# Performance work log

Measured on AMD Instinct MI355X. Metric: run time of the kernel, lower is better.

## Reference

```python
import jax, jax.numpy as jnp
import numpy as np

EPS = 1e-5

def _cfn(x, g, b):
    # ChanFreqNorm: normalize over (channel, freq) dims of [B, C, T, F]
    mu = x.mean(axis=(1, 3), keepdims=True)
    std = jnp.sqrt(((x - mu) ** 2).mean(axis=(1, 3), keepdims=True))  # unbiased=False
    return (x - mu) / (std + EPS) * g[None, :, None, :] + b[None, :, None, :]

def _branch(x, w, bi, a, g, be):
    # 1x1 conv (C_in -> C_out) + PReLU(scalar) + ChanFreqNorm
    y = jnp.einsum('bctf,oc->botf', x, w) + bi[None, :, None, None]
    y = jnp.where(y > 0, y, a * y)
    return _cfn(y, g, be)


def setup_inputs() -> dict:
    key = jax.random.key(0)
    ks = jax.random.split(key, 8)
    B, C, T, F = 8, 64, 1000, 64
    H, HS, CV = 4, 4, 16  # num_heads, hidden_size, C // num_heads
    s = 0.05
    inp = {
        'x': jax.random.normal(ks[0], (B, C, T, F), jnp.float32),
        'q_w': jax.random.normal(ks[1], (H, HS, C), jnp.float32) * s,
        'q_b': jnp.zeros((H, HS), jnp.float32),
        'q_a': jnp.full((H,), 0.25, jnp.float32),
        'q_g': jnp.ones((H, HS, F), jnp.float32),
        'q_be': jnp.zeros((H, HS, F), jnp.float32),
        'k_w': jax.random.normal(ks[2], (H, HS, C), jnp.float32) * s,
        'k_b': jnp.zeros((H, HS), jnp.float32),
        'k_a': jnp.full((H,), 0.25, jnp.float32),
        'k_g': jnp.ones((H, HS, F), jnp.float32),
        'k_be': jnp.zeros((H, HS, F), jnp.float32),
        'v_w': jax.random.normal(ks[3], (H, CV, C), jnp.float32) * s,
        'v_b': jnp.zeros((H, CV), jnp.float32),
        'v_a': jnp.full((H,), 0.25, jnp.float32),
        'v_g': jnp.ones((H, CV, F), jnp.float32),
        'v_be': jnp.zeros((H, CV, F), jnp.float32),
        'l_w': jax.random.normal(ks[4], (C, C), jnp.float32) * s,
        'l_b': jnp.zeros((C,), jnp.float32),
        'l_a': jnp.full((1,), 0.25, jnp.float32),
        'l_g': jnp.ones((C, F), jnp.float32),
        'l_be': jnp.zeros((C, F), jnp.float32),
    }
    return inp


def reference(x, q_w, q_b, q_a, q_g, q_be, k_w, k_b, k_a, k_g, k_be,
              v_w, v_b, v_a, v_g, v_be, l_w, l_b, l_a, l_g, l_be):
    B, C, T, F = x.shape
    H = q_w.shape[0]
    branch = jax.vmap(_branch, in_axes=(None, 0, 0, 0, 0, 0))
    Q = branch(x, q_w, q_b, q_a, q_g, q_be)   # [H, B, HS, T, F]
    K = branch(x, k_w, k_b, k_a, k_g, k_be)   # [H, B, HS, T, F]
    V = branch(x, v_w, v_b, v_a, v_g, v_be)   # [H, B, CV, T, F]
    HS = Q.shape[2]
    CV = V.shape[2]
    HB = H * B
    # torch.cat(dim=0) over heads == head-major reshape
    Ql = Q.reshape(HB, HS, T, F).transpose(0, 2, 1, 3).reshape(HB, T, HS * F)
    Kl = K.reshape(HB, HS, T, F).transpose(0, 2, 1, 3).reshape(HB, T, HS * F)
    Vl = V.reshape(HB, CV, T, F).transpose(0, 2, 1, 3).reshape(HB, T, CV * F)
    embed_size = H * F  # num_heads * num_freqs
    scores = jnp.einsum('ntd,nsd->nts', Ql, Kl) / jnp.sqrt(jnp.float32(embed_size))
    attn = jax.nn.softmax(scores, axis=-1)               # [HB, T, T]
    A = jnp.einsum('nts,nsd->ntd', attn, Vl)             # [HB, T, CV*F]
    A = A.reshape(HB, T, CV, F).transpose(0, 2, 1, 3)    # [HB, CV, T, F]
    xo = A.reshape(H, B, CV, T, F).transpose(1, 0, 2, 3, 4).reshape(B, C, T, F)
    y = jnp.einsum('bctf,oc->botf', xo, l_w) + l_b[None, :, None, None]
    y = jnp.where(y > 0, y, l_a[0] * y)
    y = _cfn(y, l_g, l_be)
    return y + x
```

## Files before the change

### kernel.cpp

```cpp
#include <hip/hip_runtime.h>
#include <hip/hip_bf16.h>

typedef __hip_bfloat16 bf16;
typedef __attribute__((ext_vector_type(8))) short bf16x8;
typedef __attribute__((ext_vector_type(4))) float f32x4;

#define TT 1000
#define SCALE 0.0625f
#define M0 20.0f
#define KSR 264
#define PSR 72
#define XSC 68

__device__ __forceinline__ float b2f(const bf16 v) { return __bfloat162float(v); }
__device__ __forceinline__ bf16 f2b(const float v) { return __float2bfloat16(v); }
__device__ __forceinline__ unsigned short f2bu(float v) { bf16 h = __float2bfloat16(v); return *(unsigned short*)&h; }
__device__ __forceinline__ float u2f(unsigned short u) { return __bfloat162float(*(const bf16*)&u); }

__global__ __launch_bounds__(256, 2) void k_qkv(
    const float* __restrict__ x,
    const float* __restrict__ qw, const float* __restrict__ qb, const float* __restrict__ qa,
    const float* __restrict__ qg, const float* __restrict__ qbe,
    const float* __restrict__ kw, const float* __restrict__ kb, const float* __restrict__ ka,
    const float* __restrict__ kg, const float* __restrict__ kbe,
    const float* __restrict__ vw, const float* __restrict__ vb, const float* __restrict__ va,
    const float* __restrict__ vg, const float* __restrict__ vbe,
    bf16* __restrict__ Ql, bf16* __restrict__ Kl, bf16* __restrict__ Vl)
{
    __shared__ float Xs[2][64][XSC];
    __shared__ uint4 Whs[12 * 64];
    __shared__ uint4 Wls[12 * 64];
    __shared__ float gs_s[2][12][4];
    __shared__ float gq_s[2][12][4];
    __shared__ float bias_s[96];
    __shared__ float alpha_s[24];

    const int tid  = threadIdx.x;
    const int b    = blockIdx.x / 125;
    const int ch   = blockIdx.x % 125;
    const int tb   = ch * 8;

    const int w    = tid >> 6;
    const int lane = tid & 63;
    const int cl   = lane & 15;
    const int oct  = lane >> 4;
    const int f    = w * 16 + cl;

    #pragma unroll
    for (int i = 0; i < 3; ++i) {
        const int s  = w * 3 + i;
        const int mt = s >> 1, kk = s & 1;
        const int row = mt * 16 + cl;
        const float* wp = (row < 16) ? (qw + row * 64)
                        : (row < 32) ? (kw + (row - 16) * 64)
                                     : (vw + (row - 32) * 64);
        const int c0 = kk * 32 + oct * 8;
        const float4 a0 = *(const float4*)(wp + c0);
        const float4 a1 = *(const float4*)(wp + c0 + 4);
        const float vvv[8] = {a0.x, a0.y, a0.z, a0.w, a1.x, a1.y, a1.z, a1.w};
        union { unsigned short u[8]; uint4 q; } hi, lo;
        #pragma unroll
        for (int j = 0; j < 8; ++j) {
            const unsigned short h = f2bu(vvv[j]);
            hi.u[j] = h;
            lo.u[j] = f2bu(vvv[j] - u2f(h));
        }
        Whs[s * 64 + lane] = hi.q;
        Wls[s * 64 + lane] = lo.q;
    }
    if (tid < 96) {
        const int r = tid;
        bias_s[r] = (r < 16) ? qb[r] : (r < 32) ? kb[r - 16] : vb[r - 32];
    }
    if (tid < 24) {
        const int mt = tid >> 2, oc = tid & 3;
        alpha_s[tid] = (mt == 0) ? qa[oc] : (mt == 1) ? ka[oc] : va[mt - 2];
    }

    float g_r[24], be_r[24];
    #pragma unroll
    for (int mt = 0; mt < 6; ++mt)
        #pragma unroll
        for (int r = 0; r < 4; ++r) {
            const int row = mt * 16 + oct * 4 + r;
            const float* gp; const float* bp; int rr;
            if (row < 16)      { rr = row;      gp = qg; bp = qbe; }
            else if (row < 32) { rr = row - 16; gp = kg; bp = kbe; }
            else               { rr = row - 32; gp = vg; bp = vbe; }
            g_r[mt * 4 + r]  = gp[rr * 64 + f];
            be_r[mt * 4 + r] = bp[rr * 64 + f];
        }

    auto stageX = [&](int t0) {
        const int c = lane;
        #pragma unroll
        for (int tt = 0; tt < 2; ++tt) {
            const float* xp = x + ((size_t)(b * 64 + c) * TT + (t0 + tt)) * 64 + w * 16;
            const float4 v0 = *(const float4*)(xp);
            const float4 v1 = *(const float4*)(xp + 4);
            const float4 v2 = *(const float4*)(xp + 8);
            const float4 v3 = *(const float4*)(xp + 12);
            const float vv[16] = {v0.x, v0.y, v0.z, v0.w, v1.x, v1.y, v1.z, v1.w,
                                  v2.x, v2.y, v2.z, v2.w, v3.x, v3.y, v3.z, v3.w};
            #pragma unroll
            for (int j = 0; j < 16; ++j) Xs[tt][w * 16 + j][c] = vv[j];
        }
    };

    stageX(tb);
    __syncthreads();

    for (int it = 0; it < 4; ++it) {
        const int t0 = tb + it * 2;

        f32x4 acc[2][6];
        #pragma unroll
        for (int tt = 0; tt < 2; ++tt)
            #pragma unroll
            for (int mt = 0; mt < 6; ++mt) acc[tt][mt] = (f32x4)0.f;

        #pragma unroll
        for (int tt = 0; tt < 2; ++tt) {
            #pragma unroll
            for (int kk = 0; kk < 2; ++kk) {
                const float* xr = &Xs[tt][w * 16 + cl][kk * 32 + oct * 8];
                const float4 x0 = *(const float4*)(xr);
                const float4 x1 = *(const float4*)(xr + 4);
                const float xvv[8] = {x0.x, x0.y, x0.z, x0.w, x1.x, x1.y, x1.z, x1.w};
                union { unsigned short u[8]; bf16x8 v; } xh, xl;
                #pragma unroll
                for (int j = 0; j < 8; ++j) {
                    const unsigned short h = f2bu(xvv[j]);
                    xh.u[j] = h;
                    xl.u[j] = f2bu(xvv[j] - u2f(h));
                }
                #pragma unroll
                for (int mt = 0; mt < 6; ++mt) {
                    const bf16x8 wh = *(const bf16x8*)&Whs[(mt * 2 + kk) * 64 + lane];
                    const bf16x8 wl = *(const bf16x8*)&Wls[(mt * 2 + kk) * 64 + lane];
                    acc[tt][mt] = __builtin_amdgcn_mfma_f32_16x16x32_bf16(wh, xh.v, acc[tt][mt], 0, 0, 0);
                    acc[tt][mt] = __builtin_amdgcn_mfma_f32_16x16x32_bf16(wh, xl.v, acc[tt][mt], 0, 0, 0);
                    acc[tt][mt] = __builtin_amdgcn_mfma_f32_16x16x32_bf16(wl, xh.v, acc[tt][mt], 0, 0, 0);
                }
            }
        }

        #pragma unroll
        for (int tt = 0; tt < 2; ++tt)
            #pragma unroll
            for (int mt = 0; mt < 6; ++mt) {
                float s = 0.f, q = 0.f;
                #pragma unroll
                for (int r = 0; r < 4; ++r) {
                    float v = acc[tt][mt][r] + bias_s[mt * 16 + oct * 4 + r];
                    const float a = alpha_s[mt * 4 + oct];
                    v = v > 0.f ? v : a * v;
                    acc[tt][mt][r] = v;
                    s += v; q += v * v;
                }
                s += __shfl_xor(s, 1); q += __shfl_xor(q, 1);
                s += __shfl_xor(s, 2); q += __shfl_xor(q, 2);
                s += __shfl_xor(s, 4); q += __shfl_xor(q, 4);
                s += __shfl_xor(s, 8); q += __shfl_xor(q, 8);
                if (mt < 2) {
                    if (cl == 0) { gs_s[tt][mt * 4 + oct][w] = s; gq_s[tt][mt * 4 + oct][w] = q; }
                } else {
                    s += __shfl_xor(s, 16); q += __shfl_xor(q, 16);
                    s += __shfl_xor(s, 32); q += __shfl_xor(q, 32);
                    if (lane == 0) { gs_s[tt][8 + mt - 2][w] = s; gq_s[tt][8 + mt - 2][w] = q; }
                }
            }
        __syncthreads();

        #pragma unroll
        for (int tt = 0; tt < 2; ++tt) {
            const int t = t0 + tt;
            #pragma unroll
            for (int mt = 0; mt < 6; ++mt) {
                const int g = (mt < 2) ? (mt * 4 + oct) : (8 + mt - 2);
                const float s = gs_s[tt][g][0] + gs_s[tt][g][1] + gs_s[tt][g][2] + gs_s[tt][g][3];
                const float q = gq_s[tt][g][0] + gq_s[tt][g][1] + gq_s[tt][g][2] + gq_s[tt][g][3];
                const float cnt = (mt < 2) ? 256.f : 1024.f;
                const float mu = s / cnt;
                const float var = fmaxf(q / cnt - mu * mu, 0.f);
                const float sc = 1.f / (sqrtf(var) + 1e-5f);
                #pragma unroll
                for (int r = 0; r < 4; ++r) {
                    const float out = (acc[tt][mt][r] - mu) * sc * g_r[mt * 4 + r] + be_r[mt * 4 + r];
                    if (mt == 0) {
                        Ql[((size_t)(oct * 8 + b) * TT + t) * 256 + r * 64 + f] = f2b(out);
                    } else if (mt == 1) {
                        Kl[((size_t)(oct * 8 + b) * TT + t) * 256 + r * 64 + f] = f2b(out);
                    } else {
                        Vl[((size_t)((mt - 2) * 8 + b) * TT + t) * 1024 + (oct * 4 + r) * 64 + f] = f2b(out);
                    }
                }
            }
        }

        if (it < 3) stageX(tb + (it + 1) * 2);
        __syncthreads();
    }
}

__global__ __launch_bounds__(256, 2) void k_vt(
    const unsigned short* __restrict__ Vl, unsigned short* __restrict__ Vt)
{
    __shared__ unsigned short Ts[64 * 80];
    const int tid = threadIdx.x;
    const int n  = blockIdx.x >> 8;
    const int tt = (blockIdx.x >> 4) & 15;
    const int dt = blockIdx.x & 15;
    const int t0 = tt * 64, d0 = dt * 64;

    #pragma unroll
    for (int i = 0; i < 2; ++i) {
        const int chunk = tid + i * 256;
        const int trow = chunk >> 3, tc8 = (chunk & 7) * 8;
        uint4 v = make_uint4(0u, 0u, 0u, 0u);
        const int t = t0 + trow;
        if (t < TT) v = *(const uint4*)&Vl[((size_t)n * TT + t) * 1024 + d0 + tc8];
        *(uint4*)&Ts[trow * 80 + tc8] = v;
    }
    __syncthreads();
    #pragma unroll
    for (int i = 0; i < 2; ++i) {
        const int chunk = tid + i * 256;
        const int drow = chunk >> 3, sc8 = (chunk & 7) * 8;
        union { unsigned short u[8]; uint4 v; } pk;
        #pragma unroll
        for (int j = 0; j < 8; ++j) pk.u[j] = Ts[(sc8 + j) * 80 + drow];
        *(uint4*)&Vt[((size_t)n * 1024 + d0 + drow) * 1024 + t0 + sc8] = pk.v;
    }
}

__global__ __launch_bounds__(512, 2) void k_attn(
    const unsigned short* __restrict__ Ql, const unsigned short* __restrict__ Kl,
    const unsigned short* __restrict__ Vt, bf16* __restrict__ Aout)
{
    __shared__ unsigned short Qs[64 * KSR];
    __shared__ unsigned short Ks[64 * KSR];
    __shared__ unsigned short Ps[64 * PSR];
    __shared__ float lred[8][32];
    __shared__ float invl[64];

    const int tid  = threadIdx.x;
    const int bid  = blockIdx.x;
    const int xcd  = bid & 7;
    const int r0   = bid >> 3;
    const int n    = xcd * 4 + (r0 >> 4);
    const int t0   = (r0 & 15) * 64;
    const int valid_r = TT - t0;

    const int w    = tid >> 6;
    const int lane = tid & 63;
    const int cl   = lane & 15;
    const int oct  = lane >> 4;

    const int qh   = w & 1;
    const int sw   = w >> 1;

    #pragma unroll
    for (int i = 0; i < 4; ++i) {
        const int chunk = tid + i * 512;
        const int row = chunk >> 5, c8 = (chunk & 31) * 8;
        uint4 v = make_uint4(0u, 0u, 0u, 0u);
        if (row < valid_r)
            v = *(const uint4*)&Ql[((size_t)n * TT + t0 + row) * 256 + c8];
        *(uint4*)&Qs[row * KSR + c8] = v;
    }
    #pragma unroll
    for (int i = 0; i < 4; ++i) {
        const int chunk = tid + i * 512;
        const int row = chunk >> 5, c8 = (chunk & 31) * 8;
        uint4 v = make_uint4(0u, 0u, 0u, 0u);
        if (row < TT)
            v = *(const uint4*)&Kl[((size_t)n * TT + row) * 256 + c8];
        *(uint4*)&Ks[row * KSR + c8] = v;
    }
    __syncthreads();

    f32x4 acc[4][8];
    #pragma unroll
    for (int qt = 0; qt < 4; ++qt)
        #pragma unroll
        for (int dt = 0; dt < 8; ++dt) acc[qt][dt] = (f32x4)0.f;
    float l_acc[2][4] = {{0.f,0.f,0.f,0.f},{0.f,0.f,0.f,0.f}};

    for (int ts = 0; ts < 16; ++ts) {
        const int s0 = ts * 64;

        f32x4 sacc0 = (f32x4)0.f, sacc1 = (f32x4)0.f;
        #pragma unroll
        for (int k = 0; k < 8; ++k) {
            const bf16x8 bk  = *(const bf16x8*)&Ks[(sw * 16 + cl) * KSR + k * 32 + oct * 8];
            const bf16x8 aq0 = *(const bf16x8*)&Qs[(qh * 32 + cl) * KSR + k * 32 + oct * 8];
            const bf16x8 aq1 = *(const bf16x8*)&Qs[(qh * 32 + 16 + cl) * KSR + k * 32 + oct * 8];
            sacc0 = __builtin_amdgcn_mfma_f32_16x16x32_bf16(aq0, bk, sacc0, 0, 0, 0);
            sacc1 = __builtin_amdgcn_mfma_f32_16x16x32_bf16(aq1, bk, sacc1, 0, 0, 0);
        }
        const float msk = (s0 + sw * 16 + cl < TT) ? 1.f : 0.f;
        #pragma unroll
        for (int r = 0; r < 4; ++r) {
            const float p0 = msk * __expf(sacc0[r] * SCALE - M0);
            const float p1 = msk * __expf(sacc1[r] * SCALE - M0);
            l_acc[0][r] += p0;
            l_acc[1][r] += p1;
            Ps[(qh * 32 + oct * 4 + r) * PSR + sw * 16 + cl] = f2bu(p0);
            Ps[(qh * 32 + 16 + oct * 4 + r) * PSR + sw * 16 + cl] = f2bu(p1);
        }
        __syncthreads();

        const int s0n = s0 + 64;
        uint4 kv[2];
        if (ts < 15) {
            #pragma unroll
            for (int i = 0; i < 2; ++i) {
                const int chunk = tid + i * 512;
                const int row = chunk >> 5, c8 = (chunk & 31) * 8;
                kv[i] = make_uint4(0u, 0u, 0u, 0u);
                if (s0n + row < TT)
                    kv[i] = *(const uint4*)&Kl[((size_t)n * TT + s0n + row) * 256 + c8];
            }
        }

        bf16x8 pa[4][2];
        #pragma unroll
        for (int qt = 0; qt < 4; ++qt)
            #pragma unroll
            for (int kc = 0; kc < 2; ++kc)
                pa[qt][kc] = *(const bf16x8*)&Ps[(qt * 16 + cl) * PSR + kc * 32 + oct * 8];

        const unsigned short* vbase =
            Vt + ((size_t)n * 1024 + w * 128 + cl) * 1024 + s0 + oct * 8;

        {
            bf16x8 vb[4][2];
            #pragma unroll
            for (int dt = 0; dt < 4; ++dt) {
                const unsigned short* vp = vbase + (size_t)(dt * 16) * 1024;
                vb[dt][0] = *(const bf16x8*)(vp);
                vb[dt][1] = *(const bf16x8*)(vp + 32);
            }
            #pragma unroll
            for (int dt = 0; dt < 4; ++dt)
                #pragma unroll
                for (int qt = 0; qt < 4; ++qt) {
                    acc[qt][dt] = __builtin_amdgcn_mfma_f32_16x16x32_bf16(pa[qt][0], vb[dt][0], acc[qt][dt], 0, 0, 0);
                    acc[qt][dt] = __builtin_amdgcn_mfma_f32_16x16x32_bf16(pa[qt][1], vb[dt][1], acc[qt][dt], 0, 0, 0);
                }
        }

        if (ts < 15) {
            #pragma unroll
            for (int i = 0; i < 2; ++i) {
                const int chunk = tid + i * 512;
                const int row = chunk >> 5, c8 = (chunk & 31) * 8;
                *(uint4*)&Ks[row * KSR + c8] = kv[i];
            }
            #pragma unroll
            for (int i = 2; i < 4; ++i) {
                const int chunk = tid + i * 512;
                const int row = chunk >> 5, c8 = (chunk & 31) * 8;
                kv[i - 2] = make_uint4(0u, 0u, 0u, 0u);
                if (s0n + row < TT)
                    kv[i - 2] = *(const uint4*)&Kl[((size_t)n * TT + s0n + row) * 256 + c8];
            }
        }

        {
            bf16x8 vb[4][2];
            #pragma unroll
            for (int dt = 0; dt < 4; ++dt) {
                const unsigned short* vp = vbase + (size_t)((dt + 4) * 16) * 1024;
                vb[dt][0] = *(const bf16x8*)(vp);
                vb[dt][1] = *(const bf16x8*)(vp + 32);
            }
            #pragma unroll
            for (int dt = 0; dt < 4; ++dt)
                #pragma unroll
                for (int qt = 0; qt < 4; ++qt) {
                    acc[qt][dt + 4] = __builtin_amdgcn_mfma_f32_16x16x32_bf16(pa[qt][0], vb[dt][0], acc[qt][dt + 4], 0, 0, 0);
                    acc[qt][dt + 4] = __builtin_amdgcn_mfma_f32_16x16x32_bf16(pa[qt][1], vb[dt][1], acc[qt][dt + 4], 0, 0, 0);
                }
        }

        if (ts < 15) {
            #pragma unroll
            for (int i = 2; i < 4; ++i) {
                const int chunk = tid + i * 512;
                const int row = chunk >> 5, c8 = (chunk & 31) * 8;
                *(uint4*)&Ks[row * KSR + c8] = kv[i - 2];
            }
        }
        __syncthreads();
    }

    #pragma unroll
    for (int u = 0; u < 2; ++u)
        #pragma unroll
        for (int r = 0; r < 4; ++r) {
            float l = l_acc[u][r];
            l += __shfl_xor(l, 1); l += __shfl_xor(l, 2);
            l += __shfl_xor(l, 4); l += __shfl_xor(l, 8);
            l_acc[u][r] = l;
        }
    if (cl == 0) {
        #pragma unroll
        for (int u = 0; u < 2; ++u)
            #pragma unroll
            for (int r = 0; r < 4; ++r)
                lred[w][u * 16 + oct * 4 + r] = l_acc[u][r];
    }
    __syncthreads();
    if (tid < 64) {
        const int qhh = tid >> 5, rh = tid & 31;
        invl[tid] = 1.f / (lred[qhh][rh] + lred[qhh + 2][rh] +
                           lred[qhh + 4][rh] + lred[qhh + 6][rh]);
    }
    __syncthreads();

    #pragma unroll
    for (int qt = 0; qt < 4; ++qt)
        #pragma unroll
        for (int r = 0; r < 4; ++r) {
            const int row = qt * 16 + oct * 4 + r;
            if (row < valid_r) {
                bf16* op = Aout + ((size_t)n * TT + t0 + row) * 1024 + w * 128 + cl;
                const float iv = invl[row];
                #pragma unroll
                for (int dt = 0; dt < 8; ++dt)
                    op[dt * 16] = f2b(acc[qt][dt][r] * iv);
            }
        }
}

__global__ __launch_bounds__(256, 2) void k_final(
    const bf16* __restrict__ Ain, const float* __restrict__ x,
    const float* __restrict__ lw, const float* __restrict__ lb, const float* __restrict__ la,
    const float* __restrict__ lg, const float* __restrict__ lbe,
    float* __restrict__ out)
{
    __shared__ float Xs[2][64][XSC];
    __shared__ uint4 Whs[8 * 64];
    __shared__ uint4 Wls[8 * 64];
    __shared__ float red_s[2][2][4];
    __shared__ float bias_s[64];

    const int tid  = threadIdx.x;
    const int b    = blockIdx.x / 125;
    const int ch   = blockIdx.x % 125;
    const int tb   = ch * 8;

    const int w    = tid >> 6;
    const int lane = tid & 63;
    const int cl   = lane & 15;
    const int oct  = lane >> 4;
    const int f    = w * 16 + cl;

    #pragma unroll
    for (int i = 0; i < 2; ++i) {
        const int s  = w * 2 + i;
        const int mt = s >> 1, kk = s & 1;
        const float* wp = lw + (mt * 16 + cl) * 64 + kk * 32 + oct * 8;
        const float4 a0 = *(const float4*)(wp);
        const float4 a1 = *(const float4*)(wp + 4);
        const float vvv[8] = {a0.x, a0.y, a0.z, a0.w, a1.x, a1.y, a1.z, a1.w};
        union { unsigned short u[8]; uint4 q; } hi, lo;
        #pragma unroll
        for (int j = 0; j < 8; ++j) {
            const unsigned short h = f2bu(vvv[j]);
            hi.u[j] = h;
            lo.u[j] = f2bu(vvv[j] - u2f(h));
        }
        Whs[s * 64 + lane] = hi.q;
        Wls[s * 64 + lane] = lo.q;
    }
    if (tid < 64) bias_s[tid] = lb[tid];
    const float alpha = la[0];

    float g_r[16], be_r[16];
    #pragma unroll
    for (int mt = 0; mt < 4; ++mt)
        #pragma unroll
        for (int r = 0; r < 4; ++r) {
            const int rr = mt * 16 + oct * 4 + r;
            g_r[mt * 4 + r]  = lg[rr * 64 + f];
            be_r[mt * 4 + r] = lbe[rr * 64 + f];
        }

    auto stageA = [&](int t0) {
        #pragma unroll
        for (int tt = 0; tt < 2; ++tt) {
            const int t = t0 + tt;
            #pragma unroll
            for (int i = 0; i < 2; ++i) {
                const int chunk = tid + i * 256;
                const int cch = chunk >> 3, e8 = (chunk & 7) * 8;
                const int h = cch >> 4, o = cch & 15;
                union { unsigned short u[8]; uint4 v; } pk;
                pk.v = *(const uint4*)&Ain[(size_t)((h * 8 + b) * TT + t) * 1024 + o * 64 + e8];
                #pragma unroll
                for (int j = 0; j < 8; ++j)
                    Xs[tt][e8 + j][cch] = u2f(pk.u[j]);
            }
        }
    };

    stageA(tb);
    __syncthreads();

    for (int it = 0; it < 4; ++it) {
        const int t0 = tb + it * 2;

        f32x4 acc[2][4];
        #pragma unroll
        for (int tt = 0; tt < 2; ++tt)
            #pragma unroll
            for (int mt = 0; mt < 4; ++mt) acc[tt][mt] = (f32x4)0.f;

        #pragma unroll
        for (int tt = 0; tt < 2; ++tt) {
            #pragma unroll
            for (int kk = 0; kk < 2; ++kk) {
                const float* xr = &Xs[tt][w * 16 + cl][kk * 32 + oct * 8];
                const float4 x0 = *(const float4*)(xr);
                const float4 x1 = *(const float4*)(xr + 4);
                const float xvv[8] = {x0.x, x0.y, x0.z, x0.w, x1.x, x1.y, x1.z, x1.w};
                union { unsigned short u[8]; bf16x8 v; } xb;
                #pragma unroll
                for (int j = 0; j < 8; ++j) xb.u[j] = f2bu(xvv[j]);
                #pragma unroll
                for (int mt = 0; mt < 4; ++mt) {
                    const bf16x8 wh = *(const bf16x8*)&Whs[(mt * 2 + kk) * 64 + lane];
                    const bf16x8 wl = *(const bf16x8*)&Wls[(mt * 2 + kk) * 64 + lane];
                    acc[tt][mt] = __builtin_amdgcn_mfma_f32_16x16x32_bf16(wh, xb.v, acc[tt][mt], 0, 0, 0);
                    acc[tt][mt] = __builtin_amdgcn_mfma_f32_16x16x32_bf16(wl, xb.v, acc[tt][mt], 0, 0, 0);
                }
            }
        }

        #pragma unroll
        for (int tt = 0; tt < 2; ++tt) {
            float s = 0.f, q = 0.f;
            #pragma unroll
            for (int mt = 0; mt < 4; ++mt)
                #pragma unroll
                for (int r = 0; r < 4; ++r) {
                    float v = acc[tt][mt][r] + bias_s[mt * 16 + oct * 4 + r];
                    v = v > 0.f ? v : alpha * v;
                    acc[tt][mt][r] = v;
                    s += v; q += v * v;
                }
            #pragma unroll
            for (int off = 32; off > 0; off >>= 1) {
                s += __shfl_xor(s, off);
                q += __shfl_xor(q, off);
            }
            if (lane == 0) { red_s[tt][0][w] = s; red_s[tt][1][w] = q; }
        }
        __syncthreads();

        #pragma unroll
        for (int tt = 0; tt < 2; ++tt) {
            const int t = t0 + tt;
            const float S = red_s[tt][0][0] + red_s[tt][0][1] + red_s[tt][0][2] + red_s[tt][0][3];
            const float Q = red_s[tt][1][0] + red_s[tt][1][1] + red_s[tt][1][2] + red_s[tt][1][3];
            const float mu = S / 4096.f;
            const float var = fmaxf(Q / 4096.f - mu * mu, 0.f);
            const float sc = 1.f / (sqrtf(var) + 1e-5f);
            #pragma unroll
            for (int mt = 0; mt < 4; ++mt)
                #pragma unroll
                for (int r = 0; r < 4; ++r) {
                    const int rr = mt * 16 + oct * 4 + r;
                    const size_t gi = ((size_t)(b * 64 + rr) * TT + t) * 64 + f;
                    out[gi] = (acc[tt][mt][r] - mu) * sc * g_r[mt * 4 + r]
                            + be_r[mt * 4 + r] + x[gi];
                }
        }

        if (it < 3) stageA(tb + (it + 1) * 2);
        __syncthreads();
    }
}

extern "C" void kernel_launch(void* const* d_in, const int* in_sizes, int n_in,
                              void* d_out, int out_size, void* d_ws, size_t ws_size,
                              hipStream_t stream) {
    (void)in_sizes; (void)n_in; (void)out_size; (void)ws_size;
    const float* x    = (const float*)d_in[0];
    const float* q_w  = (const float*)d_in[1];
    const float* q_b  = (const float*)d_in[2];
    const float* q_a  = (const float*)d_in[3];
    const float* q_g  = (const float*)d_in[4];
    const float* q_be = (const float*)d_in[5];
    const float* k_w  = (const float*)d_in[6];
    const float* k_b  = (const float*)d_in[7];
    const float* k_a  = (const float*)d_in[8];
    const float* k_g  = (const float*)d_in[9];
    const float* k_be = (const float*)d_in[10];
    const float* v_w  = (const float*)d_in[11];
    const float* v_b  = (const float*)d_in[12];
    const float* v_a  = (const float*)d_in[13];
    const float* v_g  = (const float*)d_in[14];
    const float* v_be = (const float*)d_in[15];
    const float* l_w  = (const float*)d_in[16];
    const float* l_b  = (const float*)d_in[17];
    const float* l_a  = (const float*)d_in[18];
    const float* l_g  = (const float*)d_in[19];
    const float* l_be = (const float*)d_in[20];

    char* ws = (char*)d_ws;
    bf16* Ql = (bf16*)(ws);
    bf16* Kl = (bf16*)(ws + 16384000);
    bf16* Vl = (bf16*)(ws + 32768000);
    bf16* Vt = (bf16*)(ws + 98304000);
    bf16* A  = (bf16*)(ws + 32768000);

    k_qkv<<<8 * 125, 256, 0, stream>>>(x,
        q_w, q_b, q_a, q_g, q_be,
        k_w, k_b, k_a, k_g, k_be,
        v_w, v_b, v_a, v_g, v_be,
        Ql, Kl, Vl);
    k_vt<<<32 * 16 * 16, 256, 0, stream>>>((const unsigned short*)Vl, (unsigned short*)Vt);
    k_attn<<<32 * 16, 512, 0, stream>>>((const unsigned short*)Ql, (const unsigned short*)Kl,
                                        (const unsigned short*)Vt, A);
    k_final<<<8 * 125, 256, 0, stream>>>(A, x, l_w, l_b, l_a, l_g, l_be, (float*)d_out);
}
```

Measured before the change: 574.8 us.

## Retile attention blocks to 128 query rows and half the value dimension

Each attention block now covers 128 query rows and half of the 1024-wide value dimension instead of 64 rows and the full width. Each warp owns 64 value columns and reuses every V register fragment across 8 query tiles, which halves V global reads per query row. The cost is that QK^T scores and softmax are computed twice, once per value half, and Q shared memory and the P tile double in size.

```diff
diff --git a/kernel.cpp b/kernel.cpp
--- a/kernel.cpp
+++ b/kernel.cpp
@@ -238,18 +238,20 @@
     const unsigned short* __restrict__ Ql, const unsigned short* __restrict__ Kl,
     const unsigned short* __restrict__ Vt, bf16* __restrict__ Aout)
 {
-    __shared__ unsigned short Qs[64 * KSR];
+    __shared__ unsigned short Qs[128 * KSR];
     __shared__ unsigned short Ks[64 * KSR];
-    __shared__ unsigned short Ps[64 * PSR];
+    __shared__ unsigned short Ps[128 * PSR];
     __shared__ float lred[8][32];
-    __shared__ float invl[64];
+    __shared__ float invl[128];
 
     const int tid  = threadIdx.x;
     const int bid  = blockIdx.x;
     const int xcd  = bid & 7;
     const int r0   = bid >> 3;
     const int n    = xcd * 4 + (r0 >> 4);
-    const int t0   = (r0 & 15) * 64;
+    const int sub  = r0 & 15;
+    const int t0   = (sub >> 1) * 128;
+    const int dh   = sub & 1;
     const int valid_r = TT - t0;
 
     const int w    = tid >> 6;
@@ -257,11 +259,11 @@
     const int cl   = lane & 15;
     const int oct  = lane >> 4;
 
-    const int qh   = w & 1;
-    const int sw   = w >> 1;
-
-    #pragma unroll
-    for (int i = 0; i < 4; ++i) {
+    const int qh   = w & 3;
+    const int sw   = w >> 2;
+
+    #pragma unroll
+    for (int i = 0; i < 8; ++i) {
         const int chunk = tid + i * 512;
         const int row = chunk >> 5, c8 = (chunk & 31) * 8;
         uint4 v = make_uint4(0u, 0u, 0u, 0u);
@@ -280,35 +282,45 @@
     }
     __syncthreads();
 
-    f32x4 acc[4][8];
-    #pragma unroll
-    for (int qt = 0; qt < 4; ++qt)
-        #pragma unroll
-        for (int dt = 0; dt < 8; ++dt) acc[qt][dt] = (f32x4)0.f;
+    f32x4 acc[8][4];
+    #pragma unroll
+    for (int qt = 0; qt < 8; ++qt)
+        #pragma unroll
+        for (int dt = 0; dt < 4; ++dt) acc[qt][dt] = (f32x4)0.f;
     float l_acc[2][4] = {{0.f,0.f,0.f,0.f},{0.f,0.f,0.f,0.f}};
 
     for (int ts = 0; ts < 16; ++ts) {
         const int s0 = ts * 64;
 
-        f32x4 sacc0 = (f32x4)0.f, sacc1 = (f32x4)0.f;
+        f32x4 sacc[2][2];
+        #pragma unroll
+        for (int u = 0; u < 2; ++u)
+            #pragma unroll
+            for (int v = 0; v < 2; ++v) sacc[u][v] = (f32x4)0.f;
         #pragma unroll
         for (int k = 0; k < 8; ++k) {
-            const bf16x8 bk  = *(const bf16x8*)&Ks[(sw * 16 + cl) * KSR + k * 32 + oct * 8];
+            const bf16x8 bk0 = *(const bf16x8*)&Ks[(sw * 32 + cl) * KSR + k * 32 + oct * 8];
+            const bf16x8 bk1 = *(const bf16x8*)&Ks[(sw * 32 + 16 + cl) * KSR + k * 32 + oct * 8];
             const bf16x8 aq0 = *(const bf16x8*)&Qs[(qh * 32 + cl) * KSR + k * 32 + oct * 8];
             const bf16x8 aq1 = *(const bf16x8*)&Qs[(qh * 32 + 16 + cl) * KSR + k * 32 + oct * 8];
-            sacc0 = __builtin_amdgcn_mfma_f32_16x16x32_bf16(aq0, bk, sacc0, 0, 0, 0);
-            sacc1 = __builtin_amdgcn_mfma_f32_16x16x32_bf16(aq1, bk, sacc1, 0, 0, 0);
-        }
-        const float msk = (s0 + sw * 16 + cl < TT) ? 1.f : 0.f;
-        #pragma unroll
-        for (int r = 0; r < 4; ++r) {
-            const float p0 = msk * __expf(sacc0[r] * SCALE - M0);
-            const float p1 = msk * __expf(sacc1[r] * SCALE - M0);
-            l_acc[0][r] += p0;
-            l_acc[1][r] += p1;
-            Ps[(qh * 32 + oct * 4 + r) * PSR + sw * 16 + cl] = f2bu(p0);
-            Ps[(qh * 32 + 16 + oct * 4 + r) * PSR + sw * 16 + cl] = f2bu(p1);
-        }
+            sacc[0][0] = __builtin_amdgcn_mfma_f32_16x16x32_bf16(aq0, bk0, sacc[0][0], 0, 0, 0);
+            sacc[0][1] = __builtin_amdgcn_mfma_f32_16x16x32_bf16(aq0, bk1, sacc[0][1], 0, 0, 0);
+            sacc[1][0] = __builtin_amdgcn_mfma_f32_16x16x32_bf16(aq1, bk0, sacc[1][0], 0, 0, 0);
+            sacc[1][1] = __builtin_amdgcn_mfma_f32_16x16x32_bf16(aq1, bk1, sacc[1][1], 0, 0, 0);
+        }
+        const float msk0 = (s0 + sw * 32 + cl < TT) ? 1.f : 0.f;
+        const float msk1 = (s0 + sw * 32 + 16 + cl < TT) ? 1.f : 0.f;
+        #pragma unroll
+        for (int u = 0; u < 2; ++u)
+            #pragma unroll
+            for (int r = 0; r < 4; ++r) {
+                const float p0 = msk0 * __expf(sacc[u][0][r] * SCALE - M0);
+                const float p1 = msk1 * __expf(sacc[u][1][r] * SCALE - M0);
+                l_acc[u][r] += p0 + p1;
+                const int prow = qh * 32 + u * 16 + oct * 4 + r;
+                Ps[prow * PSR + sw * 32 + cl] = f2bu(p0);
+                Ps[prow * PSR + sw * 32 + 16 + cl] = f2bu(p1);
+            }
         __syncthreads();
 
         const int s0n = s0 + 64;
@@ -324,30 +336,29 @@
             }
         }
 
-        bf16x8 pa[4][2];
-        #pragma unroll
-        for (int qt = 0; qt < 4; ++qt)
-            #pragma unroll
-            for (int kc = 0; kc < 2; ++kc)
-                pa[qt][kc] = *(const bf16x8*)&Ps[(qt * 16 + cl) * PSR + kc * 32 + oct * 8];
-
         const unsigned short* vbase =
-            Vt + ((size_t)n * 1024 + w * 128 + cl) * 1024 + s0 + oct * 8;
+            Vt + ((size_t)n * 1024 + dh * 512 + w * 64 + cl) * 1024 + s0 + oct * 8;
+        bf16x8 vb[4][2];
+        #pragma unroll
+        for (int dt = 0; dt < 4; ++dt) {
+            const unsigned short* vp = vbase + (size_t)(dt * 16) * 1024;
+            vb[dt][0] = *(const bf16x8*)(vp);
+            vb[dt][1] = *(const bf16x8*)(vp + 32);
+        }
 
         {
-            bf16x8 vb[4][2];
-            #pragma unroll
-            for (int dt = 0; dt < 4; ++dt) {
-                const unsigned short* vp = vbase + (size_t)(dt * 16) * 1024;
-                vb[dt][0] = *(const bf16x8*)(vp);
-                vb[dt][1] = *(const bf16x8*)(vp + 32);
-            }
+            bf16x8 pa[4][2];
+            #pragma unroll
+            for (int j = 0; j < 4; ++j)
+                #pragma unroll
+                for (int kc = 0; kc < 2; ++kc)
+                    pa[j][kc] = *(const bf16x8*)&Ps[(j * 16 + cl) * PSR + kc * 32 + oct * 8];
             #pragma unroll
             for (int dt = 0; dt < 4; ++dt)
                 #pragma unroll
-                for (int qt = 0; qt < 4; ++qt) {
-                    acc[qt][dt] = __builtin_amdgcn_mfma_f32_16x16x32_bf16(pa[qt][0], vb[dt][0], acc[qt][dt], 0, 0, 0);
-                    acc[qt][dt] = __builtin_amdgcn_mfma_f32_16x16x32_bf16(pa[qt][1], vb[dt][1], acc[qt][dt], 0, 0, 0);
+                for (int j = 0; j < 4; ++j) {
+                    acc[j][dt] = __builtin_amdgcn_mfma_f32_16x16x32_bf16(pa[j][0], vb[dt][0], acc[j][dt], 0, 0, 0);
+                    acc[j][dt] = __builtin_amdgcn_mfma_f32_16x16x32_bf16(pa[j][1], vb[dt][1], acc[j][dt], 0, 0, 0);
                 }
         }
 
@@ -369,19 +380,18 @@
         }
 
         {
-            bf16x8 vb[4][2];
-            #pragma unroll
-            for (int dt = 0; dt < 4; ++dt) {
-                const unsigned short* vp = vbase + (size_t)((dt + 4) * 16) * 1024;
-                vb[dt][0] = *(const bf16x8*)(vp);
-                vb[dt][1] = *(const bf16x8*)(vp + 32);
-            }
+            bf16x8 pa[4][2];
+            #pragma unroll
+            for (int j = 0; j < 4; ++j)
+                #pragma unroll
+                for (int kc = 0; kc < 2; ++kc)
+                    pa[j][kc] = *(const bf16x8*)&Ps[((4 + j) * 16 + cl) * PSR + kc * 32 + oct * 8];
             #pragma unroll
             for (int dt = 0; dt < 4; ++dt)
                 #pragma unroll
-                for (int qt = 0; qt < 4; ++qt) {
-                    acc[qt][dt + 4] = __builtin_amdgcn_mfma_f32_16x16x32_bf16(pa[qt][0], vb[dt][0], acc[qt][dt + 4], 0, 0, 0);
-                    acc[qt][dt + 4] = __builtin_amdgcn_mfma_f32_16x16x32_bf16(pa[qt][1], vb[dt][1], acc[qt][dt + 4], 0, 0, 0);
+                for (int j = 0; j < 4; ++j) {
+                    acc[4 + j][dt] = __builtin_amdgcn_mfma_f32_16x16x32_bf16(pa[j][0], vb[dt][0], acc[4 + j][dt], 0, 0, 0);
+                    acc[4 + j][dt] = __builtin_amdgcn_mfma_f32_16x16x32_bf16(pa[j][1], vb[dt][1], acc[4 + j][dt], 0, 0, 0);
                 }
         }
 
@@ -413,23 +423,22 @@
                 lred[w][u * 16 + oct * 4 + r] = l_acc[u][r];
     }
     __syncthreads();
-    if (tid < 64) {
+    if (tid < 128) {
         const int qhh = tid >> 5, rh = tid & 31;
-        invl[tid] = 1.f / (lred[qhh][rh] + lred[qhh + 2][rh] +
-                           lred[qhh + 4][rh] + lred[qhh + 6][rh]);
+        invl[tid] = 1.f / (lred[qhh][rh] + lred[qhh + 4][rh]);
     }
     __syncthreads();
 
     #pragma unroll
-    for (int qt = 0; qt < 4; ++qt)
+    for (int qt = 0; qt < 8; ++qt)
         #pragma unroll
         for (int r = 0; r < 4; ++r) {
             const int row = qt * 16 + oct * 4 + r;
             if (row < valid_r) {
-                bf16* op = Aout + ((size_t)n * TT + t0 + row) * 1024 + w * 128 + cl;
+                bf16* op = Aout + ((size_t)n * TT + t0 + row) * 1024 + dh * 512 + w * 64 + cl;
                 const float iv = invl[row];
                 #pragma unroll
-                for (int dt = 0; dt < 8; ++dt)
+                for (int dt = 0; dt < 4; ++dt)
                     op[dt * 16] = f2b(acc[qt][dt][r] * iv);
             }
         }
```

Result: faster. 529.6 us (-7.9%).
